# Performance work log

Hardware: AMD Instinct MI355X
Metric: run time of the kernel (lower is better)

The kernel has to match this reference:

```python
import jax, jax.numpy as jnp
import numpy as np

D_MODEL = 1024
HEADS = 16
HEAD_DIM = D_MODEL // HEADS


def setup_inputs() -> dict:
    key = jax.random.key(0)
    ks = jax.random.split(key, 9)
    s = 1.0 / np.sqrt(D_MODEL)
    inp = {
        "inputs": jax.random.normal(ks[0], (4, 2048, D_MODEL), dtype=jnp.float32),
        "Wq": jax.random.normal(ks[1], (D_MODEL, D_MODEL), dtype=jnp.float32) * s,
        "bq": jnp.zeros((D_MODEL,), dtype=jnp.float32),
        "Wk": jax.random.normal(ks[2], (D_MODEL, D_MODEL), dtype=jnp.float32) * s,
        "bk": jnp.zeros((D_MODEL,), dtype=jnp.float32),
        "Wv": jax.random.normal(ks[3], (D_MODEL, D_MODEL), dtype=jnp.float32) * s,
        "bv": jnp.zeros((D_MODEL,), dtype=jnp.float32),
        "Wo": jax.random.normal(ks[4], (D_MODEL, D_MODEL), dtype=jnp.float32) * s,
        "bo": jnp.zeros((D_MODEL,), dtype=jnp.float32),
    }
    return inp


def reference(inputs, Wq, bq, Wk, bk, Wv, bv, Wo, bo):
    bs, seq, _ = inputs.shape
    # projections -> [b, h, s, d]
    def split_heads(x):
        return x.reshape(bs, seq, HEADS, HEAD_DIM).transpose(0, 2, 1, 3)
    q = split_heads(inputs @ Wq + bq)
    k = split_heads(inputs @ Wk + bk)
    v = split_heads(inputs @ Wv + bv)
    # NOTE: original code divides by (head_dim ** 1 / 2) == head_dim/2, not sqrt(head_dim)
    scale = HEAD_DIM / 2.0
    scores = jnp.einsum("bhqd,bhkd->bhqk", q, k) / scale
    attn = jax.nn.softmax(scores, axis=-1)
    out = jnp.einsum("bhqk,bhkd->bhqd", attn, v)
    out = out.transpose(0, 2, 1, 3).reshape(bs, seq, HEADS * HEAD_DIM)
    return out @ Wo + bo
```

## Files before the change

### kernel.cpp

```cpp
#include <hip/hip_runtime.h>
#include <stdint.h>

typedef __attribute__((ext_vector_type(8))) short bf16x8;
typedef __attribute__((ext_vector_type(4))) float f32x4;
typedef __attribute__((address_space(1))) void as1_void;
typedef __attribute__((address_space(3))) void as3_void;

#define D_MODEL 1024
#define SEQ     2048
#define BATCH   4
#define HEADS   16
#define HDIM    64

#define QSCALE 0.045084220029218407f

__device__ __forceinline__ ushort f2bf(float f) {
  union { float f; unsigned u; } v; v.f = f;
  unsigned u = v.u + 0x7fffu + ((v.u >> 16) & 1u);
  return (ushort)(u >> 16);
}

__device__ __forceinline__ void gload_lds16(const void* g, void* l) {
  __builtin_amdgcn_global_load_lds((as1_void*)(uintptr_t)g, (as3_void*)l, 16, 0, 0);
}

__device__ __forceinline__ bf16x8 pack8(float a0, float a1, float a2, float a3,
                                        float a4, float a5, float a6, float a7) {
  union { uint u[4]; bf16x8 v; } x;
  x.u[0] = __builtin_amdgcn_perm(__float_as_uint(a1), __float_as_uint(a0), 0x07060302);
  x.u[1] = __builtin_amdgcn_perm(__float_as_uint(a3), __float_as_uint(a2), 0x07060302);
  x.u[2] = __builtin_amdgcn_perm(__float_as_uint(a5), __float_as_uint(a4), 0x07060302);
  x.u[3] = __builtin_amdgcn_perm(__float_as_uint(a7), __float_as_uint(a6), 0x07060302);
  return x.v;
}

__global__ void prep_kernel(const float* __restrict__ X,
                            const float* w0, const float* w1, const float* w2, const float* w3,
                            const float* __restrict__ bq, const float* __restrict__ bk,
                            const float* __restrict__ bv,
                            ushort* __restrict__ Xb, ushort* __restrict__ WT,
                            float* __restrict__ bcat) {
  __shared__ float tile[32][33];
  const int bx = blockIdx.x, t = threadIdx.x;
  if (bx < 8192) {
    int i = bx * 256 + t;
    float4 f = reinterpret_cast<const float4*>(X)[i];
    ushort4 o;
    o.x = f2bf(f.x); o.y = f2bf(f.y); o.z = f2bf(f.z); o.w = f2bf(f.w);
    reinterpret_cast<ushort4*>(Xb)[i] = o;
  } else if (bx < 12288) {
    int tz = bx - 8192;
    int z = tz >> 10;
    int xy = tz & 1023;
    int bxt = xy & 31, byt = xy >> 5;
    const float* w = (z == 0) ? w0 : (z == 1) ? w1 : (z == 2) ? w2 : w3;
    const float sc = (z == 0) ? QSCALE : 1.0f;
    ushort* o = WT + (size_t)z * D_MODEL * D_MODEL;
    int tx = t & 31, ty = t >> 5;
    int x = bxt * 32 + tx;
    int y0 = byt * 32;
    #pragma unroll
    for (int i = ty; i < 32; i += 8)
      tile[i][tx] = w[(size_t)(y0 + i) * D_MODEL + x];
    __syncthreads();
    #pragma unroll
    for (int i = ty; i < 32; i += 8)
      o[(size_t)(bxt * 32 + i) * D_MODEL + y0 + tx] = f2bf(tile[tx][i] * sc);
  } else {
    int i = (bx - 12288) * 256 + t;
    bcat[i] = (i < 1024) ? bq[i] * QSCALE : (i < 2048) ? bk[i - 1024] : bv[i - 2048];
  }
}

__global__ __launch_bounds__(256) void gemm_qkv(const ushort* __restrict__ A, const ushort* __restrict__ BT,
                                                const float* __restrict__ bias,
                                                ushort* __restrict__ Qh, ushort* __restrict__ Kh,
                                                ushort* __restrict__ Vt) {
  __shared__ __align__(16) ushort As[128 * 32];
  __shared__ __align__(16) ushort Bs[128 * 32];
  const int K = D_MODEL;
  const int tid  = threadIdx.x;
  const int w    = tid >> 6;
  const int lane = tid & 63;
  const int lo   = lane & 15, quad = lane >> 4;
  const int m0 = blockIdx.y * 128, n0 = blockIdx.x * 128;
  const int ra = lane >> 2;
  const int ca = (lane & 3) * 8;
  const int wm = (w & 1) * 64, wn = (w >> 1) * 64;

  f32x4 acc[4][4];
  #pragma unroll
  for (int i = 0; i < 4; ++i)
    #pragma unroll
    for (int j = 0; j < 4; ++j) acc[i][j] = {0.f, 0.f, 0.f, 0.f};

  for (int k0 = 0; k0 < K; k0 += 32) {
    #pragma unroll
    for (int i = 0; i < 2; ++i) {
      const int j = w * 2 + i;
      gload_lds16(A  + (size_t)(m0 + j * 16 + ra) * K + k0 + ca, &As[j * 512]);
      gload_lds16(BT + (size_t)(n0 + j * 16 + ra) * K + k0 + ca, &Bs[j * 512]);
    }
    __syncthreads();
    bf16x8 af[4], bfv[4];
    #pragma unroll
    for (int mi = 0; mi < 4; ++mi) af[mi]  = *(const bf16x8*)&As[(wm + mi * 16 + lo) * 32 + quad * 8];
    #pragma unroll
    for (int ni = 0; ni < 4; ++ni) bfv[ni] = *(const bf16x8*)&Bs[(wn + ni * 16 + lo) * 32 + quad * 8];
    #pragma unroll
    for (int mi = 0; mi < 4; ++mi)
      #pragma unroll
      for (int ni = 0; ni < 4; ++ni)
        acc[mi][ni] = __builtin_amdgcn_mfma_f32_16x16x32_bf16(af[mi], bfv[ni], acc[mi][ni], 0, 0, 0);
    __syncthreads();
  }

  if (blockIdx.x < 16) {
    #pragma unroll
    for (int ni = 0; ni < 4; ++ni) {
      const int col = n0 + wn + ni * 16 + lo;
      const float bv = bias[col];
      const int head = (col >> 6) & 15;
      const int d = col & 63;
      ushort* dst = (col < 1024) ? Qh : Kh;
      #pragma unroll
      for (int mi = 0; mi < 4; ++mi) {
        #pragma unroll
        for (int r = 0; r < 4; ++r) {
          const int row = m0 + wm + mi * 16 + quad * 4 + r;
          const int bidx = row >> 11, srow = row & 2047;
          dst[(size_t)((bidx * HEADS + head) * SEQ + srow) * HDIM + d] = f2bf(acc[mi][ni][r] + bv);
        }
      }
    }
  } else {
    #pragma unroll
    for (int ni = 0; ni < 4; ++ni) {
      const int col  = n0 + wn + ni * 16 + lo;
      const int vcol = col - 2048;
      const int hh = vcol >> 6, d = vcol & 63;
      const float bv = bias[col];
      #pragma unroll
      for (int mi = 0; mi < 4; ++mi) {
        const int base = m0 + wm + mi * 16;
        const int brow = base + quad * 4;
        const int bidx = brow >> 11;
        const int srow = brow & 2047;
        const int ck   = srow >> 6;
        const int c0   = (base & 32) + (quad << 3) + ((base >> 2) & 4);
        ushort e0 = f2bf(acc[mi][ni][0] + bv);
        ushort e1 = f2bf(acc[mi][ni][1] + bv);
        ushort e2 = f2bf(acc[mi][ni][2] + bv);
        ushort e3 = f2bf(acc[mi][ni][3] + bv);
        uint2 pk;
        pk.x = (uint)e0 | ((uint)e1 << 16);
        pk.y = (uint)e2 | ((uint)e3 << 16);
        *(uint2*)&Vt[(size_t)((bidx * HEADS + hh) * HDIM + d) * SEQ + ck * 64 + c0] = pk;
      }
    }
  }
}

__global__ __launch_bounds__(256) void gemm_bt_f32(const ushort* __restrict__ A, const ushort* __restrict__ BT,
                                                   const float* __restrict__ bias, float* __restrict__ C) {
  __shared__ __align__(16) ushort As[128 * 32];
  __shared__ __align__(16) ushort Bs[128 * 32];
  const int K = D_MODEL, N = D_MODEL;
  const int tid  = threadIdx.x;
  const int w    = tid >> 6;
  const int lane = tid & 63;
  const int lo   = lane & 15, quad = lane >> 4;
  const int m0 = blockIdx.y * 128, n0 = blockIdx.x * 128;
  const int ra = lane >> 2;
  const int ca = (lane & 3) * 8;
  const int wm = (w & 1) * 64, wn = (w >> 1) * 64;

  f32x4 acc[4][4];
  #pragma unroll
  for (int i = 0; i < 4; ++i)
    #pragma unroll
    for (int j = 0; j < 4; ++j) acc[i][j] = {0.f, 0.f, 0.f, 0.f};

  for (int k0 = 0; k0 < K; k0 += 32) {
    #pragma unroll
    for (int i = 0; i < 2; ++i) {
      const int j = w * 2 + i;
      gload_lds16(A  + (size_t)(m0 + j * 16 + ra) * K + k0 + ca, &As[j * 512]);
      gload_lds16(BT + (size_t)(n0 + j * 16 + ra) * K + k0 + ca, &Bs[j * 512]);
    }
    __syncthreads();
    bf16x8 af[4], bfv[4];
    #pragma unroll
    for (int mi = 0; mi < 4; ++mi) af[mi]  = *(const bf16x8*)&As[(wm + mi * 16 + lo) * 32 + quad * 8];
    #pragma unroll
    for (int ni = 0; ni < 4; ++ni) bfv[ni] = *(const bf16x8*)&Bs[(wn + ni * 16 + lo) * 32 + quad * 8];
    #pragma unroll
    for (int mi = 0; mi < 4; ++mi)
      #pragma unroll
      for (int ni = 0; ni < 4; ++ni)
        acc[mi][ni] = __builtin_amdgcn_mfma_f32_16x16x32_bf16(af[mi], bfv[ni], acc[mi][ni], 0, 0, 0);
    __syncthreads();
  }

  #pragma unroll
  for (int ni = 0; ni < 4; ++ni) {
    const int col = n0 + wn + ni * 16 + lo;
    const float bv = bias[col];
    #pragma unroll
    for (int mi = 0; mi < 4; ++mi) {
      #pragma unroll
      for (int r = 0; r < 4; ++r) {
        const int row = m0 + wm + mi * 16 + quad * 4 + r;
        C[(size_t)row * N + col] = acc[mi][ni][r] + bv;
      }
    }
  }
}

__global__ __launch_bounds__(256, 2) void attn_kernel(const ushort* __restrict__ Qh,
                                                      const ushort* __restrict__ Kh,
                                                      const ushort* __restrict__ Vt,
                                                      ushort* __restrict__ Og) {
  __shared__ __align__(16) ushort Ks[128 * 64];
  __shared__ __align__(16) ushort Vs[64 * 128];

  const int tid  = threadIdx.x;
  const int w    = tid >> 6, lane = tid & 63;
  const int lo   = lane & 15, quad = lane >> 4;
  const int bh = blockIdx.x;
  const int b = bh >> 4, h = bh & 15;
  const int qbase = blockIdx.y * 256 + w * 64;

  const ushort* Qbh = Qh + (size_t)bh * SEQ * HDIM;
  const ushort* Kbh = Kh + (size_t)bh * SEQ * HDIM;
  const ushort* Vbh = Vt + (size_t)bh * HDIM * SEQ;

  bf16x8 qf[4][2];
  #pragma unroll
  for (int qg = 0; qg < 4; ++qg) {
    const ushort* qp = Qbh + (size_t)(qbase + qg * 16 + lo) * HDIM + quad * 8;
    qf[qg][0] = *(const bf16x8*)(qp);
    qf[qg][1] = *(const bf16x8*)(qp + 32);
  }

  f32x4 acc[4][4];
  #pragma unroll
  for (int qg = 0; qg < 4; ++qg)
    #pragma unroll
    for (int t = 0; t < 4; ++t) acc[qg][t] = {0.f, 0.f, 0.f, 0.f};
  float lsum[4] = {0.f, 0.f, 0.f, 0.f};

  const int krow = lane >> 3;
  const int kseg = lane & 7;
  const int vrow = lane >> 4;
  const int vseg = lane & 15;

  for (int ck = 0; ck < SEQ / 128; ++ck) {
    __syncthreads();
    #pragma unroll
    for (int i = 0; i < 4; ++i) {
      const int jj = w * 4 + i;
      {
        const int r = jj * 8 + krow;
        const int gs = kseg ^ (r & 7);
        gload_lds16(Kbh + (size_t)(ck * 128 + r) * HDIM + gs * 8, &Ks[jj * 512]);
      }
      {
        const int d = jj * 4 + vrow;
        const int gs = vseg ^ (d & 15);
        gload_lds16(Vbh + (size_t)d * SEQ + ck * 128 + gs * 8, &Vs[jj * 512]);
      }
    }
    __syncthreads();

    #pragma unroll
    for (int x = 0; x < 2; ++x) {
      bf16x8 kf[4][2];
      #pragma unroll
      for (int sub = 0; sub < 4; ++sub) {
        const ushort* kr = &Ks[(x * 64 + sub * 16 + lo) * 64];
        kf[sub][0] = *(const bf16x8*)(kr + ((quad ^ (lo & 7)) * 8));
        kf[sub][1] = *(const bf16x8*)(kr + (((4 + quad) ^ (lo & 7)) * 8));
      }

      bf16x8 af[4][2];
      #pragma unroll
      for (int qg = 0; qg < 4; ++qg) {
        f32x4 s[4];
        #pragma unroll
        for (int sub = 0; sub < 4; ++sub) s[sub] = {0.f, 0.f, 0.f, 0.f};
        #pragma unroll
        for (int sub = 0; sub < 4; ++sub) {
          s[sub] = __builtin_amdgcn_mfma_f32_16x16x32_bf16(kf[sub][0], qf[qg][0], s[sub], 0, 0, 0);
          s[sub] = __builtin_amdgcn_mfma_f32_16x16x32_bf16(kf[sub][1], qf[qg][1], s[sub], 0, 0, 0);
        }
        float p[4][4];
        #pragma unroll
        for (int sub = 0; sub < 4; ++sub)
          #pragma unroll
          for (int r = 0; r < 4; ++r) p[sub][r] = __builtin_amdgcn_exp2f(s[sub][r]);
        float t0 = 0.f;
        #pragma unroll
        for (int sub = 0; sub < 4; ++sub)
          t0 += (p[sub][0] + p[sub][1]) + (p[sub][2] + p[sub][3]);
        lsum[qg] += t0;
        af[qg][0] = pack8(p[0][0], p[0][1], p[0][2], p[0][3], p[1][0], p[1][1], p[1][2], p[1][3]);
        af[qg][1] = pack8(p[2][0], p[2][1], p[2][2], p[2][3], p[3][0], p[3][1], p[3][2], p[3][3]);
      }

      #pragma unroll
      for (int t = 0; t < 4; ++t) {
        const ushort* vr = &Vs[(t * 16 + lo) * 128 + x * 0];
        #pragma unroll
        for (int hh = 0; hh < 2; ++hh) {
          bf16x8 vf = *(const bf16x8*)(vr + (((x * 8 + hh * 4 + quad) ^ lo) * 8));
          #pragma unroll
          for (int qg = 0; qg < 4; ++qg)
            acc[qg][t] = __builtin_amdgcn_mfma_f32_16x16x32_bf16(af[qg][hh], vf, acc[qg][t], 0, 0, 0);
        }
      }
    }
  }

  #pragma unroll
  for (int qg = 0; qg < 4; ++qg) {
    float v = lsum[qg];
    v += __shfl_xor(v, 16);
    v += __shfl_xor(v, 32);
    float linv[4];
    #pragma unroll
    for (int r = 0; r < 4; ++r) linv[r] = 1.0f / __shfl(v, quad * 4 + r);
    #pragma unroll
    for (int t = 0; t < 4; ++t)
      #pragma unroll
      for (int r = 0; r < 4; ++r)
        Og[(size_t)(b * SEQ + qbase + qg * 16 + quad * 4 + r) * D_MODEL + h * HDIM + t * 16 + lo] =
            f2bf(acc[qg][t][r] * linv[r]);
  }
}

extern "C" void kernel_launch(void* const* d_in, const int* in_sizes, int n_in,
                              void* d_out, int out_size, void* d_ws, size_t ws_size,
                              hipStream_t stream) {
  const float* X  = (const float*)d_in[0];
  const float* Wq = (const float*)d_in[1];
  const float* bq = (const float*)d_in[2];
  const float* Wk = (const float*)d_in[3];
  const float* bk = (const float*)d_in[4];
  const float* Wv = (const float*)d_in[5];
  const float* bv = (const float*)d_in[6];
  const float* Wo = (const float*)d_in[7];
  const float* bo = (const float*)d_in[8];
  float* out = (float*)d_out;
  char* ws = (char*)d_ws;

  ushort* Xb  = (ushort*)(ws);
  ushort* WT  = (ushort*)(ws + 16777216);
  ushort* Qhb = (ushort*)(ws + 25165824);
  ushort* Khb = (ushort*)(ws + 41943040);
  ushort* Vtb = (ushort*)(ws + 58720256);
  ushort* Ob  = (ushort*)(ws + 75497472);
  float*  bcat = (float*)(ws + 75497472);
  const int WSTRIDE = D_MODEL * D_MODEL;

  prep_kernel<<<12300, 256, 0, stream>>>(X, Wq, Wk, Wv, Wo, bq, bk, bv, Xb, WT, bcat);

  gemm_qkv<<<dim3(24, 64), 256, 0, stream>>>(Xb, WT, bcat, Qhb, Khb, Vtb);

  attn_kernel<<<dim3(BATCH * HEADS, SEQ / 256), 256, 0, stream>>>(Qhb, Khb, Vtb, Ob);

  gemm_bt_f32<<<dim3(8, 64), 256, 0, stream>>>(Ob, WT + 3 * WSTRIDE, bo, out);
}
```

Baseline: 287.1 us.

## Split attention keys across wave pairs with private per-wave LDS tiles

Each block now covers 128 queries instead of 256. Waves are paired so that each wave of a pair handles one half of the key sequence using its own private K/V LDS tiles, synchronising with only a vmcnt wait instead of block-wide barriers. Partial accumulators and row sums are combined through LDS at the end. This doubles the grid and raises the launch-bounds occupancy target to improve latency hiding and remove per-chunk barriers. The cost is that each wave now loads its own K/V with no sharing, which doubles global/LDS traffic per query, and a reduction epilogue is added.

```diff
diff --git a/kernel.cpp b/kernel.cpp
--- a/kernel.cpp
+++ b/kernel.cpp
@@ -217,19 +217,22 @@
   }
 }
 
-__global__ __launch_bounds__(256, 2) void attn_kernel(const ushort* __restrict__ Qh,
+__global__ __launch_bounds__(256, 4) void attn_kernel(const ushort* __restrict__ Qh,
                                                       const ushort* __restrict__ Kh,
                                                       const ushort* __restrict__ Vt,
                                                       ushort* __restrict__ Og) {
-  __shared__ __align__(16) ushort Ks[128 * 64];
-  __shared__ __align__(16) ushort Vs[64 * 128];
+  __shared__ __align__(16) ushort LDSbuf[4 * 4096];
 
   const int tid  = threadIdx.x;
   const int w    = tid >> 6, lane = tid & 63;
   const int lo   = lane & 15, quad = lane >> 4;
   const int bh = blockIdx.x;
   const int b = bh >> 4, h = bh & 15;
-  const int qbase = blockIdx.y * 256 + w * 64;
+  const int qbase = blockIdx.y * 128 + (w >> 1) * 64;
+  const int kb = (w & 1) * 1024;
+
+  ushort* Ks = &LDSbuf[w * 4096];
+  ushort* Vs = &LDSbuf[w * 4096 + 2048];
 
   const ushort* Qbh = Qh + (size_t)bh * SEQ * HDIM;
   const ushort* Kbh = Kh + (size_t)bh * SEQ * HDIM;
@@ -250,77 +253,82 @@
     for (int t = 0; t < 4; ++t) acc[qg][t] = {0.f, 0.f, 0.f, 0.f};
   float lsum[4] = {0.f, 0.f, 0.f, 0.f};
 
-  const int krow = lane >> 3;
-  const int kseg = lane & 7;
-  const int vrow = lane >> 4;
-  const int vseg = lane & 15;
-
-  for (int ck = 0; ck < SEQ / 128; ++ck) {
-    __syncthreads();
-    #pragma unroll
-    for (int i = 0; i < 4; ++i) {
-      const int jj = w * 4 + i;
-      {
-        const int r = jj * 8 + krow;
-        const int gs = kseg ^ (r & 7);
-        gload_lds16(Kbh + (size_t)(ck * 128 + r) * HDIM + gs * 8, &Ks[jj * 512]);
+  const int kr_ = lane >> 3, kseg = lane & 7;
+  const int vr_ = lane >> 2, vseg = lane & 3;
+
+  for (int ck = 0; ck < 32; ++ck) {
+    const int key0 = kb + ck * 32;
+    #pragma unroll
+    for (int j = 0; j < 4; ++j) {
+      const int r = j * 8 + kr_;
+      gload_lds16(Kbh + (size_t)(key0 + r) * HDIM + (kseg ^ (r & 7)) * 8, &Ks[j * 512]);
+    }
+    #pragma unroll
+    for (int j = 0; j < 4; ++j) {
+      const int d = j * 16 + vr_;
+      gload_lds16(Vbh + (size_t)d * SEQ + key0 + (vseg ^ (d & 3)) * 8, &Vs[j * 512]);
+    }
+    __asm__ volatile("s_waitcnt vmcnt(0)" ::: "memory");
+
+    bf16x8 kf[2][2];
+    #pragma unroll
+    for (int sub = 0; sub < 2; ++sub) {
+      const ushort* krow = &Ks[(sub * 16 + lo) * 64];
+      kf[sub][0] = *(const bf16x8*)(krow + ((quad ^ (lo & 7)) * 8));
+      kf[sub][1] = *(const bf16x8*)(krow + (((4 + quad) ^ (lo & 7)) * 8));
+    }
+
+    bf16x8 af[4];
+    #pragma unroll
+    for (int qg = 0; qg < 4; ++qg) {
+      f32x4 s[2];
+      s[0] = {0.f, 0.f, 0.f, 0.f};
+      s[1] = {0.f, 0.f, 0.f, 0.f};
+      #pragma unroll
+      for (int sub = 0; sub < 2; ++sub) {
+        s[sub] = __builtin_amdgcn_mfma_f32_16x16x32_bf16(kf[sub][0], qf[qg][0], s[sub], 0, 0, 0);
+        s[sub] = __builtin_amdgcn_mfma_f32_16x16x32_bf16(kf[sub][1], qf[qg][1], s[sub], 0, 0, 0);
       }
-      {
-        const int d = jj * 4 + vrow;
-        const int gs = vseg ^ (d & 15);
-        gload_lds16(Vbh + (size_t)d * SEQ + ck * 128 + gs * 8, &Vs[jj * 512]);
-      }
-    }
-    __syncthreads();
-
-    #pragma unroll
-    for (int x = 0; x < 2; ++x) {
-      bf16x8 kf[4][2];
-      #pragma unroll
-      for (int sub = 0; sub < 4; ++sub) {
-        const ushort* kr = &Ks[(x * 64 + sub * 16 + lo) * 64];
-        kf[sub][0] = *(const bf16x8*)(kr + ((quad ^ (lo & 7)) * 8));
-        kf[sub][1] = *(const bf16x8*)(kr + (((4 + quad) ^ (lo & 7)) * 8));
-      }
-
-      bf16x8 af[4][2];
-      #pragma unroll
-      for (int qg = 0; qg < 4; ++qg) {
-        f32x4 s[4];
+      float p[2][4];
+      #pragma unroll
+      for (int sub = 0; sub < 2; ++sub)
         #pragma unroll
-        for (int sub = 0; sub < 4; ++sub) s[sub] = {0.f, 0.f, 0.f, 0.f};
-        #pragma unroll
-        for (int sub = 0; sub < 4; ++sub) {
-          s[sub] = __builtin_amdgcn_mfma_f32_16x16x32_bf16(kf[sub][0], qf[qg][0], s[sub], 0, 0, 0);
-          s[sub] = __builtin_amdgcn_mfma_f32_16x16x32_bf16(kf[sub][1], qf[qg][1], s[sub], 0, 0, 0);
-        }
-        float p[4][4];
-        #pragma unroll
-        for (int sub = 0; sub < 4; ++sub)
-          #pragma unroll
-          for (int r = 0; r < 4; ++r) p[sub][r] = __builtin_amdgcn_exp2f(s[sub][r]);
-        float t0 = 0.f;
-        #pragma unroll
-        for (int sub = 0; sub < 4; ++sub)
-          t0 += (p[sub][0] + p[sub][1]) + (p[sub][2] + p[sub][3]);
-        lsum[qg] += t0;
-        af[qg][0] = pack8(p[0][0], p[0][1], p[0][2], p[0][3], p[1][0], p[1][1], p[1][2], p[1][3]);
-        af[qg][1] = pack8(p[2][0], p[2][1], p[2][2], p[2][3], p[3][0], p[3][1], p[3][2], p[3][3]);
-      }
-
-      #pragma unroll
-      for (int t = 0; t < 4; ++t) {
-        const ushort* vr = &Vs[(t * 16 + lo) * 128 + x * 0];
-        #pragma unroll
-        for (int hh = 0; hh < 2; ++hh) {
-          bf16x8 vf = *(const bf16x8*)(vr + (((x * 8 + hh * 4 + quad) ^ lo) * 8));
-          #pragma unroll
-          for (int qg = 0; qg < 4; ++qg)
-            acc[qg][t] = __builtin_amdgcn_mfma_f32_16x16x32_bf16(af[qg][hh], vf, acc[qg][t], 0, 0, 0);
-        }
-      }
-    }
-  }
+        for (int r = 0; r < 4; ++r) p[sub][r] = __builtin_amdgcn_exp2f(s[sub][r]);
+      lsum[qg] += (p[0][0] + p[0][1]) + (p[0][2] + p[0][3]) +
+                  (p[1][0] + p[1][1]) + (p[1][2] + p[1][3]);
+      af[qg] = pack8(p[0][0], p[0][1], p[0][2], p[0][3], p[1][0], p[1][1], p[1][2], p[1][3]);
+    }
+
+    #pragma unroll
+    for (int t = 0; t < 4; ++t) {
+      const int d = t * 16 + lo;
+      bf16x8 vf = *(const bf16x8*)&Vs[d * 32 + ((quad ^ (d & 3)) * 8)];
+      #pragma unroll
+      for (int qg = 0; qg < 4; ++qg)
+        acc[qg][t] = __builtin_amdgcn_mfma_f32_16x16x32_bf16(af[qg], vf, acc[qg][t], 0, 0, 0);
+    }
+  }
+
+  float* lred = (float*)&LDSbuf[(w | 1) * 4096];
+  #pragma unroll
+  for (int qg = 0; qg < 4; ++qg) {
+    __syncthreads();
+    if (w & 1) {
+      f32x4* dst = (f32x4*)(lred + lane * 16);
+      dst[0] = acc[qg][0]; dst[1] = acc[qg][1];
+      dst[2] = acc[qg][2]; dst[3] = acc[qg][3];
+      lred[1024 + lane] = lsum[qg];
+    }
+    __syncthreads();
+    if (!(w & 1)) {
+      const f32x4* src = (const f32x4*)(lred + lane * 16);
+      acc[qg][0] += src[0]; acc[qg][1] += src[1];
+      acc[qg][2] += src[2]; acc[qg][3] += src[3];
+      lsum[qg] += lred[1024 + lane];
+    }
+  }
+
+  if (w & 1) return;
 
   #pragma unroll
   for (int qg = 0; qg < 4; ++qg) {
@@ -367,7 +375,7 @@
 
   gemm_qkv<<<dim3(24, 64), 256, 0, stream>>>(Xb, WT, bcat, Qhb, Khb, Vtb);
 
-  attn_kernel<<<dim3(BATCH * HEADS, SEQ / 256), 256, 0, stream>>>(Qhb, Khb, Vtb, Ob);
+  attn_kernel<<<dim3(BATCH * HEADS, SEQ / 128), 256, 0, stream>>>(Qhb, Khb, Vtb, Ob);
 
   gemm_bt_f32<<<dim3(8, 64), 256, 0, stream>>>(Ob, WT + 3 * WSTRIDE, bo, out);
 }
```

After: 381.1 us. 1.33x slower.
